# Performance work log

Measured on AMD Instinct MI355X. Metric: run time of the kernel, lower is better.

Reference implementation:

```python
import jax, jax.numpy as jnp
import numpy as np

B, S, D, H = 4, 2048, 1024, 16
Dh = D // H
MAX_WAVELENGTH = 10000.0


def apply_rope(x, positions, head_dim):
    # x: [B, S, H, Dh], positions: [B, S]
    fraction = 2.0 * jnp.arange(head_dim // 2, dtype=jnp.float32) / head_dim
    timescale = MAX_WAVELENGTH ** fraction                     # [Dh/2]
    sinusoid = positions[..., None].astype(jnp.float32) / timescale  # [B, S, Dh/2]
    sinusoid = sinusoid[..., None, :]                          # [B, S, 1, Dh/2]
    sin, cos = jnp.sin(sinusoid), jnp.cos(sinusoid)
    first, second = jnp.split(x, 2, axis=-1)
    out = jnp.concatenate([first * cos - second * sin,
                           second * cos + first * sin], axis=-1)
    return out.astype(x.dtype)


def setup_inputs() -> dict:
    key = jax.random.key(0)
    k0, k1, k2, k3, k4 = jax.random.split(key, 5)
    inputs = jax.random.normal(k0, (B, S, D), dtype=jnp.float32)
    segment_positions = jnp.broadcast_to(jnp.arange(S, dtype=jnp.int32), (B, S))
    # causal mask, broadcastable over heads: [B, 1, S, S]
    mask = jnp.broadcast_to(jnp.tril(jnp.ones((S, S), dtype=bool))[None, None], (B, 1, S, S))
    std = 0.02
    w_q = jax.random.normal(k1, (D, H, Dh), dtype=jnp.float32) * std
    w_k = jax.random.normal(k2, (D, H, Dh), dtype=jnp.float32) * std
    w_v = jax.random.normal(k3, (D, H, Dh), dtype=jnp.float32) * std
    w_out = jax.random.normal(k4, (H, Dh, D), dtype=jnp.float32) * std
    return {"inputs": inputs, "w_q": w_q, "w_k": w_k, "w_v": w_v,
            "w_out": w_out, "segment_positions": segment_positions, "mask": mask}


def reference(inputs, w_q, w_k, w_v, w_out, segment_positions, mask):
    # QKV projections: [B, S, D] x [D, H, Dh] -> [B, S, H, Dh]
    q = jnp.einsum('bsd,dhk->bshk', inputs, w_q)
    k = jnp.einsum('bsd,dhk->bshk', inputs, w_k)
    v = jnp.einsum('bsd,dhk->bshk', inputs, w_v)
    q = apply_rope(q, segment_positions, Dh)
    k = apply_rope(k, segment_positions, Dh)
    q = q / jnp.sqrt(jnp.asarray(Dh, dtype=q.dtype))
    attn = jnp.einsum('bqhd,bkhd->bhqk', q, k)                 # [B, H, S, S]
    big_neg = jnp.finfo(attn.dtype).min
    attn = jnp.where(mask, attn, big_neg)
    attn = jax.nn.softmax(attn, axis=-1)
    x = jnp.einsum('bhqk,bkhd->bqhd', attn, v)                 # [B, S, H, Dh]
    return jnp.einsum('bqhd,hdm->bqm', x, w_out)               # [B, S, D]
```

## Files before the change

kernel.cpp:

```cpp
#include <hip/hip_runtime.h>
#include <stdint.h>
#include <math.h>

#define S_LEN 2048
#define DMODEL 1024
#define NHEAD 16
#define DHEAD 64
#define BATCH 4
#define MROWS (BATCH * S_LEN)

typedef __attribute__((ext_vector_type(8))) short bf16x8;
typedef __attribute__((ext_vector_type(4))) float f32x4;

#define MFMA16(a, b, c) __builtin_amdgcn_mfma_f32_16x16x32_bf16(a, b, c, 0, 0, 0)

__device__ __forceinline__ unsigned short f2b(float f) {
  union { float f; unsigned u; } v; v.f = f;
  unsigned u = v.u;
  return (unsigned short)((u + 0x7FFFu + ((u >> 16) & 1u)) >> 16);
}
__device__ __forceinline__ unsigned pkrn(float a, float b) {
  unsigned ua = __float_as_uint(a) + 0x8000u;
  unsigned ub = __float_as_uint(b) + 0x8000u;
  return __builtin_amdgcn_perm(ub, ua, 0x07060302);
}

__device__ __forceinline__ void async16(const void* g, void* l) {
  __builtin_amdgcn_global_load_lds((const __attribute__((address_space(1))) void*)g,
                                   (__attribute__((address_space(3))) void*)l,
                                   16, 0, 0);
}

__global__ __launch_bounds__(256) void cvt_kernel(const float4* __restrict__ in,
                                                  unsigned short* __restrict__ out,
                                                  int n4) {
  int i = blockIdx.x * 256 + threadIdx.x;
  if (i < n4) {
    float4 v = in[i];
    ushort4 o;
    o.x = f2b(v.x); o.y = f2b(v.y); o.z = f2b(v.z); o.w = f2b(v.w);
    *(ushort4*)(out + 4 * (size_t)i) = o;
  }
}

struct TP4 { const float* s[4]; unsigned short* d[4]; };
__global__ __launch_bounds__(256) void transpose_cvt4(TP4 p) {
  const float* in = p.s[blockIdx.z];
  unsigned short* out = p.d[blockIdx.z];
  __shared__ float T[64][65];
  int r0 = blockIdx.y * 64, c0 = blockIdx.x * 64;
  int t = threadIdx.x;
  int c = t & 63, rr = t >> 6;
#pragma unroll
  for (int i = 0; i < 16; i++) {
    int r = i * 4 + rr;
    T[r][c] = in[(size_t)(r0 + r) * 1024 + c0 + c];
  }
  __syncthreads();
  int r2 = t & 63, cc = t >> 6;
#pragma unroll
  for (int i = 0; i < 16; i++) {
    int c2 = i * 4 + cc;
    out[(size_t)(c0 + c2) * 1024 + r0 + r2] = f2b(T[r2][c2]);
  }
}

__global__ __launch_bounds__(256) void gemm_qkv(const unsigned short* __restrict__ A,
                                                const unsigned short* __restrict__ Bt,
                                                unsigned short* __restrict__ Qr,
                                                unsigned short* __restrict__ Kr,
                                                unsigned short* __restrict__ Vt,
                                                const int* __restrict__ pos) {
  constexpr int K = 1024;
  __shared__ unsigned short As[128 * 64];
  __shared__ unsigned short Bs[128 * 64];
  const int bm = blockIdx.y * 128, bn = blockIdx.x * 128;
  const int t = threadIdx.x;
  const int wave = t >> 6, lane = t & 63, quad = lane >> 4, l16 = lane & 15;
  const int wm = (wave >> 1) * 64, wn = (wave & 1) * 64;
  f32x4 acc[4][4] = {};
  const int srow = lane >> 3;
  const int gcol = (((lane & 7) ^ srow)) * 8;
  const unsigned short* Ag = A + (size_t)(bm + wave * 32 + srow) * K + gcol;
  const unsigned short* Bg = Bt + (size_t)(bn + wave * 32 + srow) * K + gcol;
  unsigned short* AsW = &As[(wave * 32) * 64];
  unsigned short* BsW = &Bs[(wave * 32) * 64];
  const int rsw = l16 & 7;

  for (int k0 = 0; k0 < K; k0 += 64) {
    __syncthreads();
#pragma unroll
    for (int i = 0; i < 4; i++) {
      async16(Ag + (size_t)(i * 8) * K + k0, AsW + i * 8 * 64);
      async16(Bg + (size_t)(i * 8) * K + k0, BsW + i * 8 * 64);
    }
    __syncthreads();
#pragma unroll
    for (int kk = 0; kk < 2; kk++) {
      const int sl = ((kk * 4 + quad) ^ rsw) << 3;
      bf16x8 af[4], bfr[4];
#pragma unroll
      for (int mt = 0; mt < 4; mt++)
        af[mt] = *(const bf16x8*)&As[(wm + mt * 16 + l16) * 64 + sl];
#pragma unroll
      for (int nt = 0; nt < 4; nt++)
        bfr[nt] = *(const bf16x8*)&Bs[(wn + nt * 16 + l16) * 64 + sl];
#pragma unroll
      for (int mt = 0; mt < 4; mt++)
#pragma unroll
        for (int nt = 0; nt < 4; nt++)
          acc[mt][nt] = MFMA16(af[mt], bfr[nt], acc[mt][nt]);
    }
  }

  const int cb = bn + wn;
  if (cb >= 2048) {
    const int h = (cb - 2048) >> 6;
#pragma unroll
    for (int mt = 0; mt < 4; mt++)
#pragma unroll
      for (int nt = 0; nt < 4; nt++) {
        int row = bm + wm + mt * 16 + quad * 4;
        int b = row >> 11, s = row & (S_LEN - 1);
        int dh = nt * 16 + l16;
        ushort4 w4;
        w4.x = f2b(acc[mt][nt][0]); w4.y = f2b(acc[mt][nt][1]);
        w4.z = f2b(acc[mt][nt][2]); w4.w = f2b(acc[mt][nt][3]);
        *(ushort4*)&Vt[((size_t)(b * NHEAD + h) * DHEAD + dh) * S_LEN + s] = w4;
      }
  } else {
    const bool isQ = cb < 1024;
    unsigned short* dst0 = isQ ? Qr : Kr;
    const float scl = isQ ? 0.18033688011112042f : 1.0f;
    const int h = (cb >> 6) & 15;
    const float LT = 0.28782313662425572f;
    float it0 = __expf(-(float)l16 * LT);
    float it1 = __expf(-(float)(16 + l16) * LT);
#pragma unroll
    for (int mt = 0; mt < 4; mt++) {
#pragma unroll
      for (int r = 0; r < 4; r++) {
        int row = bm + wm + mt * 16 + quad * 4 + r;
        int b = row >> 11, s = row & (S_LEN - 1);
        float p = (float)pos[row];
        float a0 = p * it0, a1 = p * it1;
        float sn0 = __sinf(a0), cs0 = __cosf(a0);
        float sn1 = __sinf(a1), cs1 = __cosf(a1);
        float x0 = acc[mt][0][r], x1 = acc[mt][1][r];
        float x2 = acc[mt][2][r], x3 = acc[mt][3][r];
        float o0 = (x0 * cs0 - x2 * sn0) * scl;
        float o2 = (x2 * cs0 + x0 * sn0) * scl;
        float o1 = (x1 * cs1 - x3 * sn1) * scl;
        float o3 = (x3 * cs1 + x1 * sn1) * scl;
        unsigned short* dst =
            dst0 + ((size_t)(b * NHEAD + h) * S_LEN + s) * DHEAD;
        dst[0 * 16 + l16] = f2b(o0);
        dst[1 * 16 + l16] = f2b(o1);
        dst[2 * 16 + l16] = f2b(o2);
        dst[3 * 16 + l16] = f2b(o3);
      }
    }
  }
}

__global__ __launch_bounds__(256) void gemm_out(const unsigned short* __restrict__ A,
                                                const unsigned short* __restrict__ Bt,
                                                float* __restrict__ C) {
  constexpr int K = 1024, N = 1024;
  __shared__ unsigned short As[128 * 64];
  __shared__ unsigned short Bs[128 * 64];
  const int bm = blockIdx.y * 128, bn = blockIdx.x * 128;
  const int t = threadIdx.x;
  const int wave = t >> 6, lane = t & 63, quad = lane >> 4, l16 = lane & 15;
  const int wm = (wave >> 1) * 64, wn = (wave & 1) * 64;
  f32x4 acc[4][4] = {};
  const int srow = lane >> 3;
  const int gcol = (((lane & 7) ^ srow)) * 8;
  const unsigned short* Ag = A + (size_t)(bm + wave * 32 + srow) * K + gcol;
  const unsigned short* Bg = Bt + (size_t)(bn + wave * 32 + srow) * K + gcol;
  unsigned short* AsW = &As[(wave * 32) * 64];
  unsigned short* BsW = &Bs[(wave * 32) * 64];
  const int rsw = l16 & 7;

  for (int k0 = 0; k0 < K; k0 += 64) {
    __syncthreads();
#pragma unroll
    for (int i = 0; i < 4; i++) {
      async16(Ag + (size_t)(i * 8) * K + k0, AsW + i * 8 * 64);
      async16(Bg + (size_t)(i * 8) * K + k0, BsW + i * 8 * 64);
    }
    __syncthreads();
#pragma unroll
    for (int kk = 0; kk < 2; kk++) {
      const int sl = ((kk * 4 + quad) ^ rsw) << 3;
      bf16x8 af[4], bfr[4];
#pragma unroll
      for (int mt = 0; mt < 4; mt++)
        af[mt] = *(const bf16x8*)&As[(wm + mt * 16 + l16) * 64 + sl];
#pragma unroll
      for (int nt = 0; nt < 4; nt++)
        bfr[nt] = *(const bf16x8*)&Bs[(wn + nt * 16 + l16) * 64 + sl];
#pragma unroll
      for (int mt = 0; mt < 4; mt++)
#pragma unroll
        for (int nt = 0; nt < 4; nt++)
          acc[mt][nt] = MFMA16(af[mt], bfr[nt], acc[mt][nt]);
    }
  }
#pragma unroll
  for (int mt = 0; mt < 4; mt++)
#pragma unroll
    for (int nt = 0; nt < 4; nt++)
#pragma unroll
      for (int r = 0; r < 4; r++) {
        int row = bm + wm + mt * 16 + quad * 4 + r;
        int col = bn + wn + nt * 16 + l16;
        C[(size_t)row * N + col] = acc[mt][nt][r];
      }
}

__global__ __launch_bounds__(256, 3) void flash_kernel(const unsigned short* __restrict__ Qr,
                                                       const unsigned short* __restrict__ Kr,
                                                       const unsigned short* __restrict__ Vt,
                                                       unsigned short* __restrict__ Xat) {
  const int idx = blockIdx.x;
  const int qt = 15 - (idx >> 6);
  const int bh = idx & 63;
  const unsigned short* Qh = Qr + (size_t)bh * S_LEN * DHEAD;
  const unsigned short* Kh = Kr + (size_t)bh * S_LEN * DHEAD;
  const unsigned short* Vh = Vt + (size_t)bh * DHEAD * S_LEN;
  __shared__ unsigned short Ks[2][64 * 64];
  __shared__ unsigned short Vs[2][64 * 64];
  __shared__ unsigned short Pt[4][16 * 64];
  const int t = threadIdx.x, wave = t >> 6, lane = t & 63;
  const int quad = lane >> 4, l16 = lane & 15;
  const int srow = lane >> 3;
  const int gcol = (((lane & 7) ^ srow)) * 8;
  const int rsw = l16 & 7;
  const int q0 = qt * 128;
  const int qrA = q0 + wave * 16 + l16;
  const int qrB = qrA + 64;

  bf16x8 qfA0 = *(const bf16x8*)(Qh + (size_t)qrA * DHEAD + quad * 8);
  bf16x8 qfA1 = *(const bf16x8*)(Qh + (size_t)qrA * DHEAD + 32 + quad * 8);
  bf16x8 qfB0 = *(const bf16x8*)(Qh + (size_t)qrB * DHEAD + quad * 8);
  bf16x8 qfB1 = *(const bf16x8*)(Qh + (size_t)qrB * DHEAD + 32 + quad * 8);

  f32x4 oA[4] = {}, oB[4] = {};
  float lA = 0.f, lB = 0.f;
  unsigned short* PtW = &Pt[wave][0];
  const int c0 = (quad ^ rsw) << 3;
  const int c1 = ((4 + quad) ^ rsw) << 3;
  const int q1b = quad >> 1, qlo4 = (quad & 1) * 4;
  const int pr = l16 * 64;

  auto stage = [&](int kt, int buf) {
    const int k0 = kt * 64;
#pragma unroll
    for (int i = 0; i < 2; i++) {
      async16(Kh + (size_t)(k0 + wave * 16 + i * 8 + srow) * DHEAD + gcol,
              &Ks[buf][(wave * 16 + i * 8) * 64]);
      async16(Vh + (size_t)(wave * 16 + i * 8 + srow) * S_LEN + k0 + gcol,
              &Vs[buf][(wave * 16 + i * 8) * 64]);
    }
  };

  auto softpv = [&](const unsigned short* V_, f32x4* sc, f32x4* o, float& l,
                    int qr_, bool diag, int k0) {
#pragma unroll
    for (int nt = 0; nt < 4; nt++) {
      float p0, p1, p2, p3;
      if (diag) {
        int kg = k0 + nt * 16 + quad * 4;
        p0 = (kg + 0 > qr_) ? 0.f : exp2f(sc[nt][0]);
        p1 = (kg + 1 > qr_) ? 0.f : exp2f(sc[nt][1]);
        p2 = (kg + 2 > qr_) ? 0.f : exp2f(sc[nt][2]);
        p3 = (kg + 3 > qr_) ? 0.f : exp2f(sc[nt][3]);
      } else {
        p0 = exp2f(sc[nt][0]);
        p1 = exp2f(sc[nt][1]);
        p2 = exp2f(sc[nt][2]);
        p3 = exp2f(sc[nt][3]);
      }
      l += (p0 + p1) + (p2 + p3);
      uint2 w; w.x = pkrn(p0, p1); w.y = pkrn(p2, p3);
      const int slot = ((nt * 2 + q1b) ^ rsw) << 3;
      *(uint2*)&PtW[pr + slot + qlo4] = w;
    }
#pragma unroll
    for (int kk = 0; kk < 2; kk++) {
      bf16x8 pb = *(const bf16x8*)&PtW[pr + (((kk * 4 + quad) ^ rsw) << 3)];
#pragma unroll
      for (int nt = 0; nt < 4; nt++) {
        bf16x8 vb = *(const bf16x8*)&V_[(nt * 16 + l16) * 64 + (kk == 0 ? c0 : c1)];
        o[nt] = MFMA16(vb, pb, o[nt]);
      }
    }
  };

  auto computeAB = [&](int cur, int k0, bool adiag) {
    const unsigned short* K_ = Ks[cur];
    const unsigned short* V_ = Vs[cur];
    f32x4 scA[4] = {}, scB[4] = {};
#pragma unroll
    for (int nt = 0; nt < 4; nt++) {
      bf16x8 kb0 = *(const bf16x8*)&K_[(nt * 16 + l16) * 64 + c0];
      bf16x8 kb1 = *(const bf16x8*)&K_[(nt * 16 + l16) * 64 + c1];
      scA[nt] = MFMA16(kb0, qfA0, scA[nt]);
      scA[nt] = MFMA16(kb1, qfA1, scA[nt]);
      scB[nt] = MFMA16(kb0, qfB0, scB[nt]);
      scB[nt] = MFMA16(kb1, qfB1, scB[nt]);
    }
    softpv(V_, scA, oA, lA, qrA, adiag, k0);
    softpv(V_, scB, oB, lB, qrB, false, k0);
  };

  stage(0, 0);
  const int kmax = 2 * qt;
  int kt = 0;
  for (; kt < kmax; kt += 2) {
    __syncthreads();
    stage(kt + 1, 1);
    computeAB(0, kt * 64, false);
    __syncthreads();
    stage(kt + 2, 0);
    computeAB(1, (kt + 1) * 64, false);
  }
  __syncthreads();
  stage(kmax + 1, 1);
  computeAB(0, kmax * 64, true);
  __syncthreads();
  {
    const unsigned short* K_ = Ks[1];
    const unsigned short* V_ = Vs[1];
    f32x4 scB[4] = {};
#pragma unroll
    for (int nt = 0; nt < 4; nt++) {
      bf16x8 kb0 = *(const bf16x8*)&K_[(nt * 16 + l16) * 64 + c0];
      bf16x8 kb1 = *(const bf16x8*)&K_[(nt * 16 + l16) * 64 + c1];
      scB[nt] = MFMA16(kb0, qfB0, scB[nt]);
      scB[nt] = MFMA16(kb1, qfB1, scB[nt]);
    }
    softpv(V_, scB, oB, lB, qrB, true, (kmax + 1) * 64);
  }

  lA += __shfl_xor(lA, 16); lA += __shfl_xor(lA, 32);
  lB += __shfl_xor(lB, 16); lB += __shfl_xor(lB, 32);
  const float ivA = 1.0f / lA, ivB = 1.0f / lB;
  const int b = bh >> 4, h = bh & 15;
  unsigned short* dA = Xat + (size_t)(b * S_LEN + qrA) * DMODEL + h * DHEAD;
  unsigned short* dB = Xat + (size_t)(b * S_LEN + qrB) * DMODEL + h * DHEAD;
#pragma unroll
  for (int nt = 0; nt < 4; nt++) {
    ushort4 wa, wb;
    wa.x = f2b(oA[nt][0] * ivA); wa.y = f2b(oA[nt][1] * ivA);
    wa.z = f2b(oA[nt][2] * ivA); wa.w = f2b(oA[nt][3] * ivA);
    wb.x = f2b(oB[nt][0] * ivB); wb.y = f2b(oB[nt][1] * ivB);
    wb.z = f2b(oB[nt][2] * ivB); wb.w = f2b(oB[nt][3] * ivB);
    *(ushort4*)(dA + nt * 16 + quad * 4) = wa;
    *(ushort4*)(dB + nt * 16 + quad * 4) = wb;
  }
}

extern "C" void kernel_launch(void* const* d_in, const int* in_sizes, int n_in,
                              void* d_out, int out_size, void* d_ws, size_t ws_size,
                              hipStream_t stream) {
  const float* x = (const float*)d_in[0];
  const float* wq = (const float*)d_in[1];
  const float* wk = (const float*)d_in[2];
  const float* wv = (const float*)d_in[3];
  const float* wo = (const float*)d_in[4];
  const int* pos = (const int*)d_in[5];
  float* out = (float*)d_out;
  char* ws = (char*)d_ws;

  const size_t EL_X = (size_t)MROWS * DMODEL;
  const size_t EL_W = (size_t)DMODEL * DMODEL;
  unsigned short* Xb = (unsigned short*)ws;
  unsigned short* Wqkv = Xb + EL_X;
  unsigned short* WoT = Wqkv + 3 * EL_W;
  unsigned short* Qr = WoT + EL_W;
  unsigned short* Kr = Qr + EL_X;
  unsigned short* Vt = Kr + EL_X;
  unsigned short* Xat = Vt + EL_X;

  cvt_kernel<<<(int)(EL_X / 4 / 256), 256, 0, stream>>>((const float4*)x, Xb,
                                                        (int)(EL_X / 4));
  TP4 tp;
  tp.s[0] = wq; tp.d[0] = Wqkv;
  tp.s[1] = wk; tp.d[1] = Wqkv + EL_W;
  tp.s[2] = wv; tp.d[2] = Wqkv + 2 * EL_W;
  tp.s[3] = wo; tp.d[3] = WoT;
  dim3 tg(16, 16, 4);
  transpose_cvt4<<<tg, 256, 0, stream>>>(tp);
  dim3 gq(24, 64);
  gemm_qkv<<<gq, 256, 0, stream>>>(Xb, Wqkv, Qr, Kr, Vt, pos);
  flash_kernel<<<1024, 256, 0, stream>>>(Qr, Kr, Vt, Xat);
  dim3 gg(8, 64);
  gemm_out<<<gg, 256, 0, stream>>>(Xat, WoT, out);
}
```

Baseline: 285.6 us.

## Balance causal flash work with paired query tiles and merge prep kernels

Flash attention blocks now each process a pair of 64-row query tiles, j and 31-j, instead of two adjacent tiles. This gives every block the same number of key tiles under the causal mask and removes the tail imbalance. The fp32-to-bf16 input conversion and the weight transpose kernels are merged into one launch to save launch overhead. The trade-off is a longer B-only loop phase with half the MFMA density per staged tile, plus more complex buffer-toggling logic.

```diff
diff --git a/kernel.cpp b/kernel.cpp
--- a/kernel.cpp
+++ b/kernel.cpp
@@ -31,25 +31,30 @@
                                    16, 0, 0);
 }
 
-__global__ __launch_bounds__(256) void cvt_kernel(const float4* __restrict__ in,
-                                                  unsigned short* __restrict__ out,
-                                                  int n4) {
-  int i = blockIdx.x * 256 + threadIdx.x;
-  if (i < n4) {
-    float4 v = in[i];
-    ushort4 o;
-    o.x = f2b(v.x); o.y = f2b(v.y); o.z = f2b(v.z); o.w = f2b(v.w);
-    *(ushort4*)(out + 4 * (size_t)i) = o;
-  }
-}
-
-struct TP4 { const float* s[4]; unsigned short* d[4]; };
-__global__ __launch_bounds__(256) void transpose_cvt4(TP4 p) {
-  const float* in = p.s[blockIdx.z];
-  unsigned short* out = p.d[blockIdx.z];
+struct PrepArgs {
+  const float4* x; unsigned short* xb; int n4; int cvtBlocks;
+  const float* s[4]; unsigned short* d[4];
+};
+__global__ __launch_bounds__(256) void prep_kernel(PrepArgs p) {
   __shared__ float T[64][65];
-  int r0 = blockIdx.y * 64, c0 = blockIdx.x * 64;
-  int t = threadIdx.x;
+  const int bid = blockIdx.x;
+  const int t = threadIdx.x;
+  if (bid < p.cvtBlocks) {
+    int i = bid * 256 + t;
+    if (i < p.n4) {
+      float4 v = p.x[i];
+      ushort4 o;
+      o.x = f2b(v.x); o.y = f2b(v.y); o.z = f2b(v.z); o.w = f2b(v.w);
+      *(ushort4*)(p.xb + 4 * (size_t)i) = o;
+    }
+    return;
+  }
+  const int tb = bid - p.cvtBlocks;
+  const int z = tb >> 8;
+  const int rem = tb & 255;
+  const int r0 = (rem >> 4) * 64, c0 = (rem & 15) * 64;
+  const float* in = p.s[z];
+  unsigned short* out = p.d[z];
   int c = t & 63, rr = t >> 6;
 #pragma unroll
   for (int i = 0; i < 16; i++) {
@@ -224,8 +229,9 @@
                                                        const unsigned short* __restrict__ Vt,
                                                        unsigned short* __restrict__ Xat) {
   const int idx = blockIdx.x;
-  const int qt = 15 - (idx >> 6);
+  const int j = idx >> 6;
   const int bh = idx & 63;
+  const int jB = 31 - j;
   const unsigned short* Qh = Qr + (size_t)bh * S_LEN * DHEAD;
   const unsigned short* Kh = Kr + (size_t)bh * S_LEN * DHEAD;
   const unsigned short* Vh = Vt + (size_t)bh * DHEAD * S_LEN;
@@ -237,9 +243,8 @@
   const int srow = lane >> 3;
   const int gcol = (((lane & 7) ^ srow)) * 8;
   const int rsw = l16 & 7;
-  const int q0 = qt * 128;
-  const int qrA = q0 + wave * 16 + l16;
-  const int qrB = qrA + 64;
+  const int qrA = j * 64 + wave * 16 + l16;
+  const int qrB = jB * 64 + wave * 16 + l16;
 
   bf16x8 qfA0 = *(const bf16x8*)(Qh + (size_t)qrA * DHEAD + quad * 8);
   bf16x8 qfA1 = *(const bf16x8*)(Qh + (size_t)qrA * DHEAD + 32 + quad * 8);
@@ -315,24 +320,9 @@
     softpv(V_, scB, oB, lB, qrB, false, k0);
   };
 
-  stage(0, 0);
-  const int kmax = 2 * qt;
-  int kt = 0;
-  for (; kt < kmax; kt += 2) {
-    __syncthreads();
-    stage(kt + 1, 1);
-    computeAB(0, kt * 64, false);
-    __syncthreads();
-    stage(kt + 2, 0);
-    computeAB(1, (kt + 1) * 64, false);
-  }
-  __syncthreads();
-  stage(kmax + 1, 1);
-  computeAB(0, kmax * 64, true);
-  __syncthreads();
-  {
-    const unsigned short* K_ = Ks[1];
-    const unsigned short* V_ = Vs[1];
+  auto computeB = [&](int cur, int k0, bool bdiag) {
+    const unsigned short* K_ = Ks[cur];
+    const unsigned short* V_ = Vs[cur];
     f32x4 scB[4] = {};
 #pragma unroll
     for (int nt = 0; nt < 4; nt++) {
@@ -341,8 +331,29 @@
       scB[nt] = MFMA16(kb0, qfB0, scB[nt]);
       scB[nt] = MFMA16(kb1, qfB1, scB[nt]);
     }
-    softpv(V_, scB, oB, lB, qrB, true, (kmax + 1) * 64);
-  }
+    softpv(V_, scB, oB, lB, qrB, bdiag, k0);
+  };
+
+  stage(0, 0);
+  int cur = 0;
+  for (int kt = 0; kt < j; ++kt) {
+    __syncthreads();
+    stage(kt + 1, cur ^ 1);
+    computeAB(cur, kt * 64, false);
+    cur ^= 1;
+  }
+  __syncthreads();
+  stage(j + 1, cur ^ 1);
+  computeAB(cur, j * 64, true);
+  cur ^= 1;
+  for (int kt = j + 1; kt < jB; ++kt) {
+    __syncthreads();
+    stage(kt + 1, cur ^ 1);
+    computeB(cur, kt * 64, false);
+    cur ^= 1;
+  }
+  __syncthreads();
+  computeB(cur, jB * 64, true);
 
   lA += __shfl_xor(lA, 16); lA += __shfl_xor(lA, 32);
   lB += __shfl_xor(lB, 16); lB += __shfl_xor(lB, 32);
@@ -384,15 +395,16 @@
   unsigned short* Vt = Kr + EL_X;
   unsigned short* Xat = Vt + EL_X;
 
-  cvt_kernel<<<(int)(EL_X / 4 / 256), 256, 0, stream>>>((const float4*)x, Xb,
-                                                        (int)(EL_X / 4));
-  TP4 tp;
-  tp.s[0] = wq; tp.d[0] = Wqkv;
-  tp.s[1] = wk; tp.d[1] = Wqkv + EL_W;
-  tp.s[2] = wv; tp.d[2] = Wqkv + 2 * EL_W;
-  tp.s[3] = wo; tp.d[3] = WoT;
-  dim3 tg(16, 16, 4);
-  transpose_cvt4<<<tg, 256, 0, stream>>>(tp);
+  PrepArgs pa;
+  pa.x = (const float4*)x; pa.xb = Xb;
+  pa.n4 = (int)(EL_X / 4);
+  pa.cvtBlocks = (int)(EL_X / 4 / 256);
+  pa.s[0] = wq; pa.d[0] = Wqkv;
+  pa.s[1] = wk; pa.d[1] = Wqkv + EL_W;
+  pa.s[2] = wv; pa.d[2] = Wqkv + 2 * EL_W;
+  pa.s[3] = wo; pa.d[3] = WoT;
+  prep_kernel<<<pa.cvtBlocks + 1024, 256, 0, stream>>>(pa);
+
   dim3 gq(24, 64);
   gemm_qkv<<<gq, 256, 0, stream>>>(Xb, Wqkv, Qr, Kr, Vt, pos);
   flash_kernel<<<1024, 256, 0, stream>>>(Qr, Kr, Vt, Xat);
```

Result: slower. 299.0 us (+4.7%).
